# Kernel optimization log

Hardware: AMD Instinct MI355X
Metric: run time of the kernel (lower is better)

Reference implementation:

```python
import jax, jax.numpy as jnp
import numpy as np

N_NODES = 50000
N_EDGES = 1000000
D = 66
NEG_SLOPE = 0.2
EPS_BN = 1e-5


def _glorot(key, shape):
    fan = sum(shape)
    lim = jnp.sqrt(6.0 / fan)
    return jax.random.uniform(key, shape, jnp.float32, -lim, lim)


def setup_inputs() -> dict:
    key = jax.random.key(0)
    ks = jax.random.split(key, 40)
    inp = {
        'h': jax.random.normal(ks[0], (N_NODES, D), jnp.float32),
        'edge_index': jax.random.randint(ks[1], (2, N_EDGES), 0, N_NODES, jnp.int32),
        'edge_weight': jax.random.uniform(ks[2], (N_EDGES, 1), jnp.float32),
        'bn_gamma': jnp.ones((D,), jnp.float32),
        'bn_beta': jnp.zeros((D,), jnp.float32),
    }
    i = 3
    for l in (1, 2, 3):
        inp[f'W{l}'] = _glorot(ks[i], (D, D)); i += 1
        inp[f'b{l}'] = jnp.zeros((D,), jnp.float32)
        inp[f'att_src{l}'] = _glorot(ks[i], (D,)); i += 1
        inp[f'att_dst{l}'] = _glorot(ks[i], (D,)); i += 1
        inp[f'We{l}'] = _glorot(ks[i], (1, D)); i += 1
        inp[f'att_e{l}'] = _glorot(ks[i], (D,)); i += 1
    dims = [(D, D), (D, D), (D, D), (D, D), (D, 22)]
    for l, (din, dout) in enumerate(dims, start=1):
        inp[f'fc{l}_w'] = _glorot(ks[i], (din, dout)); i += 1
        inp[f'fc{l}_b'] = jnp.zeros((dout,), jnp.float32)
    return inp


def _gat_conv(h, src, dst, edge_weight, W, b, att_src, att_dst, We, att_e):
    x = h @ W                                     # [N, D]
    a_src = x @ att_src                           # [N]
    a_dst = x @ att_dst                           # [N]
    a_e = (edge_weight @ We) @ att_e              # [E]
    alpha = a_src[src] + a_dst[dst] + a_e         # [E]
    alpha = jnp.where(alpha > 0, alpha, NEG_SLOPE * alpha)
    # scatter-softmax over destination nodes
    m = jax.ops.segment_max(alpha, dst, num_segments=N_NODES)
    m = jnp.where(jnp.isfinite(m), m, 0.0)
    ex = jnp.exp(alpha - m[dst])
    denom = jax.ops.segment_sum(ex, dst, num_segments=N_NODES)
    coef = ex / (denom[dst] + 1e-16)              # [E]
    out = jax.ops.segment_sum(coef[:, None] * x[src], dst, num_segments=N_NODES)
    return out + b


def reference(h, edge_index, edge_weight, bn_gamma, bn_beta,
              W1, b1, att_src1, att_dst1, We1, att_e1,
              W2, b2, att_src2, att_dst2, We2, att_e2,
              W3, b3, att_src3, att_dst3, We3, att_e3,
              fc1_w, fc1_b, fc2_w, fc2_b, fc3_w, fc3_b,
              fc4_w, fc4_b, fc5_w, fc5_b):
    src, dst = edge_index[0], edge_index[1]
    # BatchNorm1d (training-mode batch statistics, biased variance)
    mean = h.mean(0)
    var = ((h - mean) ** 2).mean(0)
    x = (h - mean) * jax.lax.rsqrt(var + EPS_BN) * bn_gamma + bn_beta
    x = jax.nn.relu(_gat_conv(x, src, dst, edge_weight, W1, b1, att_src1, att_dst1, We1, att_e1))
    x = jax.nn.relu(_gat_conv(x, src, dst, edge_weight, W2, b2, att_src2, att_dst2, We2, att_e2))
    x = jax.nn.relu(_gat_conv(x, src, dst, edge_weight, W3, b3, att_src3, att_dst3, We3, att_e3))
    x = jax.nn.relu(x @ fc1_w + fc1_b)
    x = jax.nn.relu(x @ fc2_w + fc2_b)
    x = jax.nn.relu(x @ fc3_w + fc3_b)
    x = jax.nn.relu(x @ fc4_w + fc4_b)
    return x @ fc5_w + fc5_b
```

## Files before the change

### kernel.cpp

```cpp
#include <hip/hip_runtime.h>
#include <math.h>

#define D 66
#define SP 68
#define NEG_SLOPE 0.2f
#define CAP 6144

typedef short s8v __attribute__((ext_vector_type(8)));
typedef float f4v __attribute__((ext_vector_type(4)));

__device__ __forceinline__ float lrelu(float a){ return a > 0.f ? a : NEG_SLOPE * a; }
__device__ __forceinline__ void fma4(float4& a, float s, const float4& w){
  a.x = fmaf(s, w.x, a.x); a.y = fmaf(s, w.y, a.y);
  a.z = fmaf(s, w.z, a.z); a.w = fmaf(s, w.w, a.w);
}
__device__ __forceinline__ unsigned short bf16r(float f){
  unsigned u = __float_as_uint(f);
  u += 0x7FFFu + ((u >> 16) & 1u);
  return (unsigned short)(u >> 16);
}
__device__ __forceinline__ float bf16f(unsigned short b){
  return __uint_as_float(((unsigned)b) << 16);
}
__device__ __forceinline__ void split8(const float* p, s8v& a0, s8v& a1, s8v& a2){
  #pragma unroll
  for (int j = 0; j < 8; j++){
    float v = p[j];
    unsigned short b0 = bf16r(v);  float f0 = bf16f(b0);
    float r1 = v - f0;
    unsigned short b1 = bf16r(r1); float f1 = bf16f(b1);
    unsigned short b2 = bf16r(r1 - f1);
    a0[j] = (short)b0; a1[j] = (short)b1; a2[j] = (short)b2;
  }
}
#define MM6(acc, a0, a1, a2, b0v, b1v, b2v)                                \
  acc = __builtin_amdgcn_mfma_f32_16x16x32_bf16(a0, b0v, acc, 0, 0, 0);    \
  acc = __builtin_amdgcn_mfma_f32_16x16x32_bf16(a1, b0v, acc, 0, 0, 0);    \
  acc = __builtin_amdgcn_mfma_f32_16x16x32_bf16(a0, b1v, acc, 0, 0, 0);    \
  acc = __builtin_amdgcn_mfma_f32_16x16x32_bf16(a2, b0v, acc, 0, 0, 0);    \
  acc = __builtin_amdgcn_mfma_f32_16x16x32_bf16(a1, b1v, acc, 0, 0, 0);    \
  acc = __builtin_amdgcn_mfma_f32_16x16x32_bf16(a0, b2v, acc, 0, 0, 0);

__global__ __launch_bounds__(256) void k_bn_stats(const float* __restrict__ h,
                                                  float* __restrict__ sums, int n){
  __shared__ float ls[2 * D];
  int t = threadIdx.x;
  if (t < 2 * D) ls[t] = 0.f;
  __syncthreads();
  int rpb = (n + gridDim.x - 1) / gridDim.x;
  int r0 = blockIdx.x * rpb;
  int r1 = min(n, r0 + rpb);
  if (t < 3 * D){
    int c = t % D, seg = t / D;
    float s1 = 0.f, s2 = 0.f;
    for (int r = r0 + seg; r < r1; r += 3){
      float v = h[(size_t)r * D + c];
      s1 += v; s2 += v * v;
    }
    atomicAdd(&ls[c], s1);
    atomicAdd(&ls[D + c], s2);
  }
  __syncthreads();
  if (t < 2 * D) atomicAdd(&sums[t], ls[t]);
}

__global__ void k_bn_finalize(const float* __restrict__ sums,
                              const float* __restrict__ gamma, const float* __restrict__ beta,
                              const float* __restrict__ We1, const float* __restrict__ ae1,
                              const float* __restrict__ We2, const float* __restrict__ ae2,
                              const float* __restrict__ We3, const float* __restrict__ ae3,
                              float* __restrict__ misc, int n){
  int t = threadIdx.x;
  if (t < D){
    float mean = sums[t] / (float)n;
    float var  = sums[D + t] / (float)n - mean * mean;
    float inv  = rsqrtf(var + 1e-5f);
    float sc = gamma[t] * inv;
    misc[t] = sc;
    misc[D + t] = beta[t] - mean * sc;
  } else if (t == D){
    float c = 0.f; for (int d = 0; d < D; d++) c += We1[d] * ae1[d]; misc[2*D + 0] = c;
  } else if (t == D + 1){
    float c = 0.f; for (int d = 0; d < D; d++) c += We2[d] * ae2[d]; misc[2*D + 1] = c;
  } else if (t == D + 2){
    float c = 0.f; for (int d = 0; d < D; d++) c += We3[d] * ae3[d]; misc[2*D + 2] = c;
  }
}

__global__ __launch_bounds__(256) void k_bn_apply(const float* __restrict__ h, const float* __restrict__ misc,
                                                  float* __restrict__ x, int n){
  int i = blockIdx.x * 256 + threadIdx.x;
  int r = i / (SP/2), c2 = i - r * (SP/2);
  if (r >= n) return;
  int c = 2 * c2;
  float2 v = make_float2(0.f, 0.f);
  if (c < D){
    float2 hv = *(const float2*)&h[(size_t)r * D + c];
    v.x = hv.x * misc[c]     + misc[D + c];
    v.y = hv.y * misc[c + 1] + misc[D + c + 1];
  }
  *(float2*)&x[(size_t)r * SP + c] = v;
}

__global__ __launch_bounds__(256) void k_pack(const float* __restrict__ w0, const float* __restrict__ w1,
                                              const float* __restrict__ w2,
                                              short* __restrict__ W0, short* __restrict__ W1,
                                              short* __restrict__ W2){
  int tid = blockIdx.x * 256 + threadIdx.x;
  if (tid >= 3 * 15 * 64) return;
  int L = tid & 63;
  int ct = (tid >> 6) % 15;
  int lay = tid / 960;
  const float* w = (lay == 0) ? w0 : ((lay == 1) ? w1 : w2);
  int c = ct / 5, t = ct % 5;
  int nn = t * 16 + (L & 15);
  int kb = c * 32 + (L >> 4) * 8;
  #pragma unroll
  for (int j = 0; j < 8; j++){
    int k = kb + j;
    float v = (k < D && nn < D) ? w[k * D + nn] : 0.f;
    unsigned short b0 = bf16r(v);  float f0 = bf16f(b0);
    float r1 = v - f0;
    unsigned short b1 = bf16r(r1); float f1 = bf16f(b1);
    unsigned short b2 = bf16r(r1 - f1);
    W0[tid * 8 + j] = (short)b0;
    W1[tid * 8 + j] = (short)b1;
    W2[tid * 8 + j] = (short)b2;
  }
}

__global__ __launch_bounds__(256) void k_packfc(const float* __restrict__ w0, const float* __restrict__ w1,
                                                const float* __restrict__ w2, const float* __restrict__ w3,
                                                const float* __restrict__ w4,
                                                const float* __restrict__ b0, const float* __restrict__ b1,
                                                const float* __restrict__ b2, const float* __restrict__ b3,
                                                const float* __restrict__ b4,
                                                short* __restrict__ W0, short* __restrict__ W1,
                                                short* __restrict__ W2, float* __restrict__ bpack){
  int tid = blockIdx.x * 256 + threadIdx.x;
  if (tid < 5 * 15 * 64){
    int L = tid & 63;
    int ct = (tid >> 6) % 15;
    int lay = tid / 960;
    const float* w = (lay == 0) ? w0 : (lay == 1) ? w1 : (lay == 2) ? w2 : (lay == 3) ? w3 : w4;
    int ncol = (lay == 4) ? 22 : D;
    int c = ct / 5, t = ct % 5;
    int nn = t * 16 + (L & 15);
    int kb = c * 32 + (L >> 4) * 8;
    #pragma unroll
    for (int j = 0; j < 8; j++){
      int k = kb + j;
      float v = (k < D && nn < ncol) ? w[k * ncol + nn] : 0.f;
      unsigned short bb0 = bf16r(v);  float f0 = bf16f(bb0);
      float r1 = v - f0;
      unsigned short bb1 = bf16r(r1); float f1 = bf16f(bb1);
      unsigned short bb2 = bf16r(r1 - f1);
      W0[tid * 8 + j] = (short)bb0;
      W1[tid * 8 + j] = (short)bb1;
      W2[tid * 8 + j] = (short)bb2;
    }
  } else if (tid < 5 * 15 * 64 + 400){
    int i = tid - 5 * 15 * 64;
    int lay = i / 80, col = i % 80;
    const float* b = (lay == 0) ? b0 : (lay == 1) ? b1 : (lay == 2) ? b2 : (lay == 3) ? b3 : b4;
    int ncol = (lay == 4) ? 22 : D;
    bpack[i] = (col < ncol) ? b[col] : 0.f;
  }
}

__global__ __launch_bounds__(256) void k_hist(const int* __restrict__ dst,
                                              int* __restrict__ bhist, int E){
  __shared__ int h[256];
  int t = threadIdx.x;
  h[t] = 0;
  __syncthreads();
  int stride = gridDim.x * blockDim.x;
  for (int e = blockIdx.x * blockDim.x + t; e < E; e += stride)
    atomicAdd(&h[dst[e] >> 8], 1);
  __syncthreads();
  if (h[t]) atomicAdd(&bhist[t], h[t]);
}

__global__ void k_bscan(const int* __restrict__ bhist, int* __restrict__ bbase,
                        int* __restrict__ gcur, int* __restrict__ rowptr, int N, int E){
  __shared__ int sh[256];
  int t = threadIdx.x;
  int v = bhist[t];
  sh[t] = v; __syncthreads();
  for (int o = 1; o < 256; o <<= 1){
    int u = (t >= o) ? sh[t - o] : 0;
    __syncthreads();
    sh[t] += u;
    __syncthreads();
  }
  int ex = sh[t] - v;
  bbase[t] = ex;
  gcur[t] = ex;
  if (t == 255){ bbase[256] = sh[255]; rowptr[N] = E; }
}

#define PCHUNK 4096
__global__ __launch_bounds__(256) void k_part(const int* __restrict__ src, const int* __restrict__ dst,
                                              const float* __restrict__ ew,
                                              int* __restrict__ gcur, int2* __restrict__ tmp, int E){
  __shared__ int hist[256];
  __shared__ int base[256];
  int t = threadIdx.x;
  int e0 = blockIdx.x * PCHUNK;
  int eend = min(E, e0 + PCHUNK);
  hist[t] = 0;
  __syncthreads();
  for (int e = e0 + t; e < eend; e += 256)
    atomicAdd(&hist[dst[e] >> 8], 1);
  __syncthreads();
  if (hist[t] > 0) base[t] = atomicAdd(&gcur[t], hist[t]);
  hist[t] = 0;
  __syncthreads();
  for (int e = e0 + t; e < eend; e += 256){
    int d = dst[e];
    int b = d >> 8;
    int off = atomicAdd(&hist[b], 1);
    tmp[base[b] + off] = make_int2((src[e] & 0xffff) | ((d & 255) << 16), __float_as_int(ew[e]));
  }
}

__global__ __launch_bounds__(256) void k_bsort(const int2* __restrict__ tmp, const int* __restrict__ bbase,
                                               int2* __restrict__ epair, int* __restrict__ rowptr, int N){
  __shared__ int2 ebuf[CAP];
  __shared__ int lcnt[256];
  __shared__ int sc[256];
  __shared__ int lcur[256];
  int b = blockIdx.x, t = threadIdx.x;
  int s0 = bbase[b], s1 = bbase[b + 1];
  int cnt = s1 - s0;
  lcnt[t] = 0;
  __syncthreads();
  for (int j = t; j < cnt; j += 256){
    int2 e = tmp[s0 + j];
    if (j < CAP) ebuf[j] = e;
    atomicAdd(&lcnt[(e.x >> 16) & 255], 1);
  }
  __syncthreads();
  int v = lcnt[t];
  sc[t] = v; __syncthreads();
  for (int o = 1; o < 256; o <<= 1){
    int u = (t >= o) ? sc[t - o] : 0;
    __syncthreads();
    sc[t] += u;
    __syncthreads();
  }
  int ex = sc[t] - v;
  int node = (b << 8) + t;
  if (node < N) rowptr[node] = s0 + ex;
  lcur[t] = ex;
  __syncthreads();
  for (int j = t; j < cnt; j += 256){
    int2 e = (j < CAP) ? ebuf[j] : tmp[s0 + j];
    int i = (e.x >> 16) & 255;
    int p = atomicAdd(&lcur[i], 1);
    epair[s0 + p] = make_int2(e.x & 0xffff, e.y);
  }
}

__global__ __launch_bounds__(256) void k_mm(const float* __restrict__ X,
    const short* __restrict__ W0, const short* __restrict__ W1, const short* __restrict__ W2,
    const float* __restrict__ att_s, const float* __restrict__ att_d,
    float* __restrict__ Y, float* __restrict__ a_src, float* __restrict__ a_dst, int n){
  const int wv = threadIdx.x >> 6, L = threadIdx.x & 63;
  const int quad = L >> 4, m = L & 15;
  const int row0 = blockIdx.x * 64 + wv * 16;
  const int lrow = min(row0 + m, n - 1);
  const float* xr = X + (size_t)lrow * SP;
  f4v acc[5];
  #pragma unroll
  for (int t = 0; t < 5; t++) acc[t] = (f4v){0.f,0.f,0.f,0.f};

  #pragma unroll
  for (int c = 0; c < 3; c++){
    float xv[8];
    if (c < 2){
      float4 p0 = *(const float4*)&xr[c * 32 + quad * 8];
      float4 p1 = *(const float4*)&xr[c * 32 + quad * 8 + 4];
      xv[0] = p0.x; xv[1] = p0.y; xv[2] = p0.z; xv[3] = p0.w;
      xv[4] = p1.x; xv[5] = p1.y; xv[6] = p1.z; xv[7] = p1.w;
    } else {
      float4 p0 = make_float4(0.f, 0.f, 0.f, 0.f);
      if (quad == 0) p0 = *(const float4*)&xr[64];
      xv[0] = p0.x; xv[1] = p0.y; xv[2] = p0.z; xv[3] = p0.w;
      xv[4] = 0.f; xv[5] = 0.f; xv[6] = 0.f; xv[7] = 0.f;
    }
    s8v a0, a1, a2;
    split8(xv, a0, a1, a2);
    const short* b0p = W0 + (c * 5) * 512 + L * 8;
    const short* b1p = W1 + (c * 5) * 512 + L * 8;
    const short* b2p = W2 + (c * 5) * 512 + L * 8;
    #pragma unroll
    for (int t = 0; t < 5; t++){
      s8v b0v = *(const s8v*)(b0p + t * 512);
      s8v b1v = *(const s8v*)(b1p + t * 512);
      s8v b2v = *(const s8v*)(b2p + t * 512);
      MM6(acc[t], a0, a1, a2, b0v, b1v, b2v)
    }
  }

  float ps[4] = {0.f,0.f,0.f,0.f}, pd[4] = {0.f,0.f,0.f,0.f};
  #pragma unroll
  for (int t = 0; t < 5; t++){
    int col = t * 16 + m;
    float as_v = 0.f, ad_v = 0.f;
    if (col < D){ as_v = att_s[col]; ad_v = att_d[col]; }
    #pragma unroll
    for (int r = 0; r < 4; r++){
      ps[r] += acc[t][r] * as_v;
      pd[r] += acc[t][r] * ad_v;
    }
  }
  #pragma unroll
  for (int r = 0; r < 4; r++){
    int rw = row0 + quad * 4 + r;
    if (rw < n){
      float* yr = Y + (size_t)rw * SP;
      #pragma unroll
      for (int t = 0; t < 4; t++) yr[t * 16 + m] = acc[t][r];
      if (m < 4) yr[64 + m] = (m < 2) ? acc[4][r] : 0.f;
    }
  }
  #pragma unroll
  for (int o = 1; o <= 8; o <<= 1){
    #pragma unroll
    for (int r = 0; r < 4; r++){
      ps[r] += __shfl_xor(ps[r], o);
      pd[r] += __shfl_xor(pd[r], o);
    }
  }
  if (m == 0){
    #pragma unroll
    for (int r = 0; r < 4; r++){
      int rw = row0 + quad * 4 + r;
      if (rw < n){ a_src[rw] = ps[r]; a_dst[rw] = pd[r]; }
    }
  }
}

#define FST 84
__global__ __launch_bounds__(256) void k_fcmm(const float* __restrict__ X,
    const short* __restrict__ W0, const short* __restrict__ W1, const short* __restrict__ W2,
    const float* __restrict__ bpack, float* __restrict__ out, int n){
  __shared__ __align__(16) float xs[4][16][FST];
  const int wv = threadIdx.x >> 6, L = threadIdx.x & 63;
  const int quad = L >> 4, m = L & 15;
  const int row0 = blockIdx.x * 64 + wv * 16;
  const int lrow = min(row0 + m, n - 1);
  const float* xr = X + (size_t)lrow * SP;

  for (int l = 0; l < 5; l++){
    const int NTl = (l == 4) ? 2 : 5;
    f4v acc[5];
    #pragma unroll
    for (int t = 0; t < 5; t++) acc[t] = (f4v){0.f,0.f,0.f,0.f};
    #pragma unroll
    for (int c = 0; c < 3; c++){
      float xv[8];
      if (l == 0){
        if (c < 2){
          float4 p0 = *(const float4*)&xr[c * 32 + quad * 8];
          float4 p1 = *(const float4*)&xr[c * 32 + quad * 8 + 4];
          xv[0] = p0.x; xv[1] = p0.y; xv[2] = p0.z; xv[3] = p0.w;
          xv[4] = p1.x; xv[5] = p1.y; xv[6] = p1.z; xv[7] = p1.w;
        } else {
          float4 p0 = make_float4(0.f, 0.f, 0.f, 0.f);
          if (quad == 0) p0 = *(const float4*)&xr[64];
          xv[0] = p0.x; xv[1] = p0.y; xv[2] = p0.z; xv[3] = p0.w;
          xv[4] = 0.f; xv[5] = 0.f; xv[6] = 0.f; xv[7] = 0.f;
        }
      } else {
        if (c == 2 && quad >= 2){
          #pragma unroll
          for (int j = 0; j < 8; j++) xv[j] = 0.f;
        } else {
          float4 p0 = *(const float4*)&xs[wv][m][c * 32 + quad * 8];
          float4 p1 = *(const float4*)&xs[wv][m][c * 32 + quad * 8 + 4];
          xv[0] = p0.x; xv[1] = p0.y; xv[2] = p0.z; xv[3] = p0.w;
          xv[4] = p1.x; xv[5] = p1.y; xv[6] = p1.z; xv[7] = p1.w;
        }
      }
      s8v a0, a1, a2;
      split8(xv, a0, a1, a2);
      const short* b0p = W0 + ((l * 3 + c) * 5) * 512 + L * 8;
      const short* b1p = W1 + ((l * 3 + c) * 5) * 512 + L * 8;
      const short* b2p = W2 + ((l * 3 + c) * 5) * 512 + L * 8;
      for (int t = 0; t < NTl; t++){
        s8v b0v = *(const s8v*)(b0p + t * 512);
        s8v b1v = *(const s8v*)(b1p + t * 512);
        s8v b2v = *(const s8v*)(b2p + t * 512);
        MM6(acc[t], a0, a1, a2, b0v, b1v, b2v)
      }
    }
    if (l < 4){
      __syncthreads();
      #pragma unroll
      for (int t = 0; t < 5; t++){
        int col = t * 16 + m;
        float bv = bpack[l * 80 + col];
        #pragma unroll
        for (int r = 0; r < 4; r++){
          float v = acc[t][r] + bv;
          xs[wv][quad * 4 + r][col] = v > 0.f ? v : 0.f;
        }
      }
      __syncthreads();
    } else {
      #pragma unroll
      for (int t = 0; t < 2; t++){
        int col = t * 16 + m;
        #pragma unroll
        for (int r = 0; r < 4; r++){
          int rw = row0 + quad * 4 + r;
          if (col < 22 && rw < n) out[(size_t)rw * 22 + col] = acc[t][r] + bpack[4 * 80 + col];
        }
      }
    }
  }
}

__global__ __launch_bounds__(256) void k_agg(const float* __restrict__ y,
                                             const float* __restrict__ a_src, const float* __restrict__ a_dst,
                                             const int* __restrict__ rowptr, const int2* __restrict__ epair,
                                             const float* __restrict__ misc, int cidx,
                                             const float* __restrict__ bias,
                                             float* __restrict__ xout, int n){
  const int wid  = (int)((blockIdx.x * (size_t)blockDim.x + threadIdx.x) >> 6);
  const int lane = threadIdx.x & 63;
  if (wid >= n) return;
  const int beg = rowptr[wid];
  const int deg = rowptr[wid + 1] - beg;
  const float ce  = misc[2 * D + cidx];
  const float adn = a_dst[wid];
  const int g = lane >> 3, q = lane & 7;

  float4 accA = make_float4(0.f,0.f,0.f,0.f);
  float4 accB = make_float4(0.f,0.f,0.f,0.f);
  float2 tacc = make_float2(0.f,0.f);

  if (deg <= 64){
    int s = 0; float al = -INFINITY;
    bool act = lane < deg;
    if (act){
      int2 ep = epair[beg + lane];
      s = ep.x;
      al = lrelu(a_src[s] + adn + ce * __int_as_float(ep.y));
    }
    float mx = al;
    #pragma unroll
    for (int o = 32; o; o >>= 1) mx = fmaxf(mx, __shfl_xor(mx, o));
    float ex = act ? __expf(al - mx) : 0.f;
    float sum = ex;
    #pragma unroll
    for (int o = 32; o; o >>= 1) sum += __shfl_xor(sum, o);
    float coef = ex * (1.f / (sum + 1e-16f));
    for (int e0 = 0; e0 < deg; e0 += 8){
      int e = e0 + g;
      int   st = __shfl(s, e);
      float ct = __shfl(coef, e);
      if (e < deg){
        const float* row = y + (size_t)st * SP;
        float4 y0 = *(const float4*)&row[4 * q];
        float4 y1 = *(const float4*)&row[32 + 4 * q];
        fma4(accA, ct, y0);
        fma4(accB, ct, y1);
        if (q == 0){
          float2 tv = *(const float2*)&row[64];
          tacc.x += ct * tv.x; tacc.y += ct * tv.y;
        }
      }
    }
  } else {
    float mx = -INFINITY;
    for (int j0 = 0; j0 < deg; j0 += 64){
      int j = j0 + lane;
      if (j < deg){
        int2 ep = epair[beg + j];
        mx = fmaxf(mx, lrelu(a_src[ep.x] + adn + ce * __int_as_float(ep.y)));
      }
    }
    #pragma unroll
    for (int o = 32; o; o >>= 1) mx = fmaxf(mx, __shfl_xor(mx, o));
    float sum = 0.f;
    for (int j0 = 0; j0 < deg; j0 += 64){
      int j = j0 + lane;
      if (j < deg){
        int2 ep = epair[beg + j];
        sum += __expf(lrelu(a_src[ep.x] + adn + ce * __int_as_float(ep.y)) - mx);
      }
    }
    #pragma unroll
    for (int o = 32; o; o >>= 1) sum += __shfl_xor(sum, o);
    float inv = 1.f / (sum + 1e-16f);
    for (int j0 = 0; j0 < deg; j0 += 64){
      int cnt = min(64, deg - j0);
      int s = 0; float ex = 0.f;
      if (lane < cnt){
        int2 ep = epair[beg + j0 + lane];
        s = ep.x;
        ex = __expf(lrelu(a_src[s] + adn + ce * __int_as_float(ep.y)) - mx);
      }
      float coef = ex * inv;
      for (int e0 = 0; e0 < cnt; e0 += 8){
        int e = e0 + g;
        int   st = __shfl(s, e);
        float ct = __shfl(coef, e);
        if (e < cnt){
          const float* row = y + (size_t)st * SP;
          float4 y0 = *(const float4*)&row[4 * q];
          float4 y1 = *(const float4*)&row[32 + 4 * q];
          fma4(accA, ct, y0);
          fma4(accB, ct, y1);
          if (q == 0){
            float2 tv = *(const float2*)&row[64];
            tacc.x += ct * tv.x; tacc.y += ct * tv.y;
          }
        }
      }
    }
  }

  #pragma unroll
  for (int o = 8; o <= 32; o <<= 1){
    accA.x += __shfl_xor(accA.x, o); accA.y += __shfl_xor(accA.y, o);
    accA.z += __shfl_xor(accA.z, o); accA.w += __shfl_xor(accA.w, o);
    accB.x += __shfl_xor(accB.x, o); accB.y += __shfl_xor(accB.y, o);
    accB.z += __shfl_xor(accB.z, o); accB.w += __shfl_xor(accB.w, o);
    tacc.x += __shfl_xor(tacc.x, o); tacc.y += __shfl_xor(tacc.y, o);
  }
  float* orow = xout + (size_t)wid * SP;
  if (lane < 8){
    float4 v;
    v.x = accA.x + bias[4*lane+0]; v.x = v.x > 0.f ? v.x : 0.f;
    v.y = accA.y + bias[4*lane+1]; v.y = v.y > 0.f ? v.y : 0.f;
    v.z = accA.z + bias[4*lane+2]; v.z = v.z > 0.f ? v.z : 0.f;
    v.w = accA.w + bias[4*lane+3]; v.w = v.w > 0.f ? v.w : 0.f;
    *(float4*)&orow[4 * lane] = v;
  } else if (lane < 16){
    int qq = lane - 8;
    float4 v;
    v.x = accB.x + bias[32+4*qq+0]; v.x = v.x > 0.f ? v.x : 0.f;
    v.y = accB.y + bias[32+4*qq+1]; v.y = v.y > 0.f ? v.y : 0.f;
    v.z = accB.z + bias[32+4*qq+2]; v.z = v.z > 0.f ? v.z : 0.f;
    v.w = accB.w + bias[32+4*qq+3]; v.w = v.w > 0.f ? v.w : 0.f;
    *(float4*)&orow[32 + 4 * qq] = v;
  }
  if (lane == 0){
    float4 tv;
    tv.x = tacc.x + bias[64]; tv.x = tv.x > 0.f ? tv.x : 0.f;
    tv.y = tacc.y + bias[65]; tv.y = tv.y > 0.f ? tv.y : 0.f;
    tv.z = 0.f; tv.w = 0.f;
    *(float4*)&orow[64] = tv;
  }
}

extern "C" void kernel_launch(void* const* d_in, const int* in_sizes, int n_in,
                              void* d_out, int out_size, void* d_ws, size_t ws_size,
                              hipStream_t stream){
  const float* h     = (const float*)d_in[0];
  const int*   ei    = (const int*)  d_in[1];
  const float* ew    = (const float*)d_in[2];
  const float* gamma = (const float*)d_in[3];
  const float* beta  = (const float*)d_in[4];
  const float *Wl[3], *bl[3], *asl[3], *adl[3], *Wel[3], *ael[3];
  int idx = 5;
  for (int l = 0; l < 3; l++){
    Wl[l]  = (const float*)d_in[idx++];
    bl[l]  = (const float*)d_in[idx++];
    asl[l] = (const float*)d_in[idx++];
    adl[l] = (const float*)d_in[idx++];
    Wel[l] = (const float*)d_in[idx++];
    ael[l] = (const float*)d_in[idx++];
  }
  const float *fw[5], *fb[5];
  for (int l = 0; l < 5; l++){ fw[l] = (const float*)d_in[idx++]; fb[l] = (const float*)d_in[idx++]; }

  int N = in_sizes[0] / D;
  int E = in_sizes[1] / 2;
  const int* src  = ei;
  const int* dstp = ei + E;

  char* base = (char*)d_ws;
  size_t o = 0;
  auto alloc = [&](size_t b){ size_t r = o; o += (b + 255) & ~(size_t)255; return r; };
  float*  bufA   = (float*)(base + alloc((size_t)N * SP * 4));
  float*  bufB   = (float*)(base + alloc((size_t)N * SP * 4));
  float*  a_src  = (float*)(base + alloc((size_t)N * 4));
  float*  a_dst  = (float*)(base + alloc((size_t)N * 4));
  float*  misc   = (float*)(base + alloc(512 * 4));
  float*  sums   = (float*)(base + alloc(2 * D * 4));
  int*    rowptr = (int*)  (base + alloc((size_t)(N + 1) * 4));
  int*    bhist  = (int*)  (base + alloc(256 * 4));
  int*    bbase  = (int*)  (base + alloc(257 * 4));
  int*    gcur   = (int*)  (base + alloc(256 * 4));
  int2*   epair  = (int2*) (base + alloc((size_t)E * 8));
  short*  W0p    = (short*)(base + alloc(3 * 7680 * 2));
  short*  W1p    = (short*)(base + alloc(3 * 7680 * 2));
  short*  W2p    = (short*)(base + alloc(3 * 7680 * 2));
  short*  FW0p   = (short*)(base + alloc(5 * 7680 * 2));
  short*  FW1p   = (short*)(base + alloc(5 * 7680 * 2));
  short*  FW2p   = (short*)(base + alloc(5 * 7680 * 2));
  float*  bpack  = (float*)(base + alloc(400 * 4));
  int2*   tmp    = (int2*)bufB;

  hipMemsetAsync(sums, 0, 2 * D * 4, stream);
  hipMemsetAsync(bhist, 0, 256 * 4, stream);

  k_bn_stats<<<256, 256, 0, stream>>>(h, sums, N);
  k_bn_finalize<<<1, 128, 0, stream>>>(sums, gamma, beta, Wel[0], ael[0], Wel[1], ael[1], Wel[2], ael[2], misc, N);
  k_pack<<<12, 256, 0, stream>>>(Wl[0], Wl[1], Wl[2], W0p, W1p, W2p);
  k_packfc<<<21, 256, 0, stream>>>(fw[0], fw[1], fw[2], fw[3], fw[4],
                                   fb[0], fb[1], fb[2], fb[3], fb[4],
                                   FW0p, FW1p, FW2p, bpack);

  int NB = (N + 255) >> 8;
  k_hist<<<256, 256, 0, stream>>>(dstp, bhist, E);
  k_bscan<<<1, 256, 0, stream>>>(bhist, bbase, gcur, rowptr, N, E);
  k_part<<<(E + PCHUNK - 1) / PCHUNK, 256, 0, stream>>>(src, dstp, ew, gcur, tmp, E);
  k_bsort<<<NB, 256, 0, stream>>>(tmp, bbase, epair, rowptr, N);

  int bnb = ((size_t)N * (SP/2) + 255) / 256;
  k_bn_apply<<<bnb, 256, 0, stream>>>(h, misc, bufA, N);

  int gb = (N + 63) / 64;
  int ab = (N + 3) / 4;

  for (int l = 0; l < 3; l++){
    k_mm<<<gb, 256, 0, stream>>>(bufA, W0p + l * 7680, W1p + l * 7680, W2p + l * 7680,
                                 asl[l], adl[l], bufB, a_src, a_dst, N);
    k_agg<<<ab, 256, 0, stream>>>(bufB, a_src, a_dst, rowptr, epair, misc, l, bl[l], bufA, N);
  }

  k_fcmm<<<gb, 256, 0, stream>>>(bufA, FW0p, FW1p, FW2p, bpack, (float*)d_out, N);
}
```

Baseline: 475.4 us.

## Fuse prep kernels, fold BatchNorm into first matmul, truncate-split activations

BN stats and the dst histogram now run as one launch, and BN finalize plus both weight-packing steps share a single prep kernel, which removes several small launches. The BN apply kernel is gone; the first GAT matmul reads raw h and applies the scale and shift inline, so one full pass over the node features is no longer written and re-read. Activations are split into three bf16 parts by truncation instead of round-to-nearest, which needs fewer ALU ops but leaves larger residuals for the lower parts. In the FC kernel the block barriers around the per-wave shared-memory exchange become a compiler memory fence, which relies on each wave touching only its own slice.

```diff
diff --git a/kernel.cpp b/kernel.cpp
--- a/kernel.cpp
+++ b/kernel.cpp
@@ -22,15 +22,18 @@
 __device__ __forceinline__ float bf16f(unsigned short b){
   return __uint_as_float(((unsigned)b) << 16);
 }
-__device__ __forceinline__ void split8(const float* p, s8v& a0, s8v& a1, s8v& a2){
+__device__ __forceinline__ void split8t(const float* p, s8v& a0, s8v& a1, s8v& a2){
   #pragma unroll
   for (int j = 0; j < 8; j++){
     float v = p[j];
-    unsigned short b0 = bf16r(v);  float f0 = bf16f(b0);
-    float r1 = v - f0;
-    unsigned short b1 = bf16r(r1); float f1 = bf16f(b1);
-    unsigned short b2 = bf16r(r1 - f1);
-    a0[j] = (short)b0; a1[j] = (short)b1; a2[j] = (short)b2;
+    unsigned u0 = __float_as_uint(v) & 0xFFFF0000u;
+    float r1 = v - __uint_as_float(u0);
+    unsigned u1 = __float_as_uint(r1) & 0xFFFF0000u;
+    float r2 = r1 - __uint_as_float(u1);
+    unsigned u2 = __float_as_uint(r2);
+    a0[j] = (short)(u0 >> 16);
+    a1[j] = (short)(u1 >> 16);
+    a2[j] = (short)(u2 >> 16);
   }
 }
 #define MM6(acc, a0, a1, a2, b0v, b1v, b2v)                                \
@@ -41,144 +44,118 @@
   acc = __builtin_amdgcn_mfma_f32_16x16x32_bf16(a1, b1v, acc, 0, 0, 0);    \
   acc = __builtin_amdgcn_mfma_f32_16x16x32_bf16(a0, b2v, acc, 0, 0, 0);
 
-__global__ __launch_bounds__(256) void k_bn_stats(const float* __restrict__ h,
-                                                  float* __restrict__ sums, int n){
-  __shared__ float ls[2 * D];
+__global__ __launch_bounds__(256) void k_stats_hist(const float* __restrict__ h, const int* __restrict__ dst,
+                                                    float* __restrict__ sums, int* __restrict__ bhist,
+                                                    int n, int E){
   int t = threadIdx.x;
-  if (t < 2 * D) ls[t] = 0.f;
-  __syncthreads();
-  int rpb = (n + gridDim.x - 1) / gridDim.x;
-  int r0 = blockIdx.x * rpb;
-  int r1 = min(n, r0 + rpb);
-  if (t < 3 * D){
-    int c = t % D, seg = t / D;
-    float s1 = 0.f, s2 = 0.f;
-    for (int r = r0 + seg; r < r1; r += 3){
-      float v = h[(size_t)r * D + c];
-      s1 += v; s2 += v * v;
-    }
-    atomicAdd(&ls[c], s1);
-    atomicAdd(&ls[D + c], s2);
-  }
-  __syncthreads();
-  if (t < 2 * D) atomicAdd(&sums[t], ls[t]);
-}
-
-__global__ void k_bn_finalize(const float* __restrict__ sums,
-                              const float* __restrict__ gamma, const float* __restrict__ beta,
-                              const float* __restrict__ We1, const float* __restrict__ ae1,
-                              const float* __restrict__ We2, const float* __restrict__ ae2,
-                              const float* __restrict__ We3, const float* __restrict__ ae3,
-                              float* __restrict__ misc, int n){
+  if (blockIdx.x < 256){
+    __shared__ float ls[2 * D];
+    if (t < 2 * D) ls[t] = 0.f;
+    __syncthreads();
+    int rpb = (n + 255) / 256;
+    int r0 = blockIdx.x * rpb;
+    int r1 = min(n, r0 + rpb);
+    if (t < 3 * D){
+      int c = t % D, seg = t / D;
+      float s1 = 0.f, s2 = 0.f;
+      for (int r = r0 + seg; r < r1; r += 3){
+        float v = h[(size_t)r * D + c];
+        s1 += v; s2 += v * v;
+      }
+      atomicAdd(&ls[c], s1);
+      atomicAdd(&ls[D + c], s2);
+    }
+    __syncthreads();
+    if (t < 2 * D) atomicAdd(&sums[t], ls[t]);
+  } else {
+    __shared__ int hh[256];
+    hh[t] = 0;
+    __syncthreads();
+    int stride = 256 * 256;
+    for (int e = (blockIdx.x - 256) * 256 + t; e < E; e += stride)
+      atomicAdd(&hh[dst[e] >> 8], 1);
+    __syncthreads();
+    if (hh[t]) atomicAdd(&bhist[t], hh[t]);
+  }
+}
+
+struct PrepArgs {
+  const float *sums, *gamma, *beta;
+  const float *We[3], *ae[3];
+  const float *gw[3];
+  const float *fw[5], *fb[5];
+  float *misc; short *W0, *W1, *W2; short *F0, *F1, *F2; float *bpack;
+  int n;
+};
+
+__global__ __launch_bounds__(256) void k_prep(PrepArgs pa){
   int t = threadIdx.x;
-  if (t < D){
-    float mean = sums[t] / (float)n;
-    float var  = sums[D + t] / (float)n - mean * mean;
-    float inv  = rsqrtf(var + 1e-5f);
-    float sc = gamma[t] * inv;
-    misc[t] = sc;
-    misc[D + t] = beta[t] - mean * sc;
-  } else if (t == D){
-    float c = 0.f; for (int d = 0; d < D; d++) c += We1[d] * ae1[d]; misc[2*D + 0] = c;
-  } else if (t == D + 1){
-    float c = 0.f; for (int d = 0; d < D; d++) c += We2[d] * ae2[d]; misc[2*D + 1] = c;
-  } else if (t == D + 2){
-    float c = 0.f; for (int d = 0; d < D; d++) c += We3[d] * ae3[d]; misc[2*D + 2] = c;
-  }
-}
-
-__global__ __launch_bounds__(256) void k_bn_apply(const float* __restrict__ h, const float* __restrict__ misc,
-                                                  float* __restrict__ x, int n){
-  int i = blockIdx.x * 256 + threadIdx.x;
-  int r = i / (SP/2), c2 = i - r * (SP/2);
-  if (r >= n) return;
-  int c = 2 * c2;
-  float2 v = make_float2(0.f, 0.f);
-  if (c < D){
-    float2 hv = *(const float2*)&h[(size_t)r * D + c];
-    v.x = hv.x * misc[c]     + misc[D + c];
-    v.y = hv.y * misc[c + 1] + misc[D + c + 1];
-  }
-  *(float2*)&x[(size_t)r * SP + c] = v;
-}
-
-__global__ __launch_bounds__(256) void k_pack(const float* __restrict__ w0, const float* __restrict__ w1,
-                                              const float* __restrict__ w2,
-                                              short* __restrict__ W0, short* __restrict__ W1,
-                                              short* __restrict__ W2){
-  int tid = blockIdx.x * 256 + threadIdx.x;
-  if (tid >= 3 * 15 * 64) return;
-  int L = tid & 63;
-  int ct = (tid >> 6) % 15;
-  int lay = tid / 960;
-  const float* w = (lay == 0) ? w0 : ((lay == 1) ? w1 : w2);
-  int c = ct / 5, t = ct % 5;
-  int nn = t * 16 + (L & 15);
-  int kb = c * 32 + (L >> 4) * 8;
-  #pragma unroll
-  for (int j = 0; j < 8; j++){
-    int k = kb + j;
-    float v = (k < D && nn < D) ? w[k * D + nn] : 0.f;
-    unsigned short b0 = bf16r(v);  float f0 = bf16f(b0);
-    float r1 = v - f0;
-    unsigned short b1 = bf16r(r1); float f1 = bf16f(b1);
-    unsigned short b2 = bf16r(r1 - f1);
-    W0[tid * 8 + j] = (short)b0;
-    W1[tid * 8 + j] = (short)b1;
-    W2[tid * 8 + j] = (short)b2;
-  }
-}
-
-__global__ __launch_bounds__(256) void k_packfc(const float* __restrict__ w0, const float* __restrict__ w1,
-                                                const float* __restrict__ w2, const float* __restrict__ w3,
-                                                const float* __restrict__ w4,
-                                                const float* __restrict__ b0, const float* __restrict__ b1,
-                                                const float* __restrict__ b2, const float* __restrict__ b3,
-                                                const float* __restrict__ b4,
-                                                short* __restrict__ W0, short* __restrict__ W1,
-                                                short* __restrict__ W2, float* __restrict__ bpack){
-  int tid = blockIdx.x * 256 + threadIdx.x;
-  if (tid < 5 * 15 * 64){
+  if (blockIdx.x == 0){
+    if (t < D){
+      float mean = pa.sums[t] / (float)pa.n;
+      float var  = pa.sums[D + t] / (float)pa.n - mean * mean;
+      float inv  = rsqrtf(var + 1e-5f);
+      float sc = pa.gamma[t] * inv;
+      pa.misc[t] = sc;
+      pa.misc[D + t] = pa.beta[t] - mean * sc;
+    } else if (t >= D && t < D + 3){
+      int l = t - D;
+      float c = 0.f;
+      for (int d = 0; d < D; d++) c += pa.We[l][d] * pa.ae[l][d];
+      pa.misc[2 * D + l] = c;
+    }
+  } else if (blockIdx.x <= 12){
+    int tid = (blockIdx.x - 1) * 256 + t;
+    if (tid >= 3 * 960) return;
     int L = tid & 63;
     int ct = (tid >> 6) % 15;
     int lay = tid / 960;
-    const float* w = (lay == 0) ? w0 : (lay == 1) ? w1 : (lay == 2) ? w2 : (lay == 3) ? w3 : w4;
-    int ncol = (lay == 4) ? 22 : D;
-    int c = ct / 5, t = ct % 5;
-    int nn = t * 16 + (L & 15);
+    const float* w = pa.gw[lay];
+    int c = ct / 5, tt = ct % 5;
+    int nn = tt * 16 + (L & 15);
     int kb = c * 32 + (L >> 4) * 8;
     #pragma unroll
     for (int j = 0; j < 8; j++){
       int k = kb + j;
-      float v = (k < D && nn < ncol) ? w[k * ncol + nn] : 0.f;
-      unsigned short bb0 = bf16r(v);  float f0 = bf16f(bb0);
+      float v = (k < D && nn < D) ? w[k * D + nn] : 0.f;
+      unsigned short b0 = bf16r(v);  float f0 = bf16f(b0);
       float r1 = v - f0;
-      unsigned short bb1 = bf16r(r1); float f1 = bf16f(bb1);
-      unsigned short bb2 = bf16r(r1 - f1);
-      W0[tid * 8 + j] = (short)bb0;
-      W1[tid * 8 + j] = (short)bb1;
-      W2[tid * 8 + j] = (short)bb2;
-    }
-  } else if (tid < 5 * 15 * 64 + 400){
-    int i = tid - 5 * 15 * 64;
-    int lay = i / 80, col = i % 80;
-    const float* b = (lay == 0) ? b0 : (lay == 1) ? b1 : (lay == 2) ? b2 : (lay == 3) ? b3 : b4;
-    int ncol = (lay == 4) ? 22 : D;
-    bpack[i] = (col < ncol) ? b[col] : 0.f;
-  }
-}
-
-__global__ __launch_bounds__(256) void k_hist(const int* __restrict__ dst,
-                                              int* __restrict__ bhist, int E){
-  __shared__ int h[256];
-  int t = threadIdx.x;
-  h[t] = 0;
-  __syncthreads();
-  int stride = gridDim.x * blockDim.x;
-  for (int e = blockIdx.x * blockDim.x + t; e < E; e += stride)
-    atomicAdd(&h[dst[e] >> 8], 1);
-  __syncthreads();
-  if (h[t]) atomicAdd(&bhist[t], h[t]);
+      unsigned short b1 = bf16r(r1); float f1 = bf16f(b1);
+      unsigned short b2 = bf16r(r1 - f1);
+      pa.W0[tid * 8 + j] = (short)b0;
+      pa.W1[tid * 8 + j] = (short)b1;
+      pa.W2[tid * 8 + j] = (short)b2;
+    }
+  } else {
+    int tid = (blockIdx.x - 13) * 256 + t;
+    if (tid < 5 * 960){
+      int L = tid & 63;
+      int ct = (tid >> 6) % 15;
+      int lay = tid / 960;
+      const float* w = pa.fw[lay];
+      int ncol = (lay == 4) ? 22 : D;
+      int c = ct / 5, tt = ct % 5;
+      int nn = tt * 16 + (L & 15);
+      int kb = c * 32 + (L >> 4) * 8;
+      #pragma unroll
+      for (int j = 0; j < 8; j++){
+        int k = kb + j;
+        float v = (k < D && nn < ncol) ? w[k * ncol + nn] : 0.f;
+        unsigned short b0 = bf16r(v);  float f0 = bf16f(b0);
+        float r1 = v - f0;
+        unsigned short b1 = bf16r(r1); float f1 = bf16f(b1);
+        unsigned short b2 = bf16r(r1 - f1);
+        pa.F0[tid * 8 + j] = (short)b0;
+        pa.F1[tid * 8 + j] = (short)b1;
+        pa.F2[tid * 8 + j] = (short)b2;
+      }
+    } else if (tid < 5 * 960 + 400){
+      int i = tid - 5 * 960;
+      int lay = i / 80, col = i % 80;
+      int ncol = (lay == 4) ? 22 : D;
+      pa.bpack[i] = (col < ncol) ? pa.fb[lay][col] : 0.f;
+    }
+  }
 }
 
 __global__ void k_bscan(const int* __restrict__ bhist, int* __restrict__ bbase,
@@ -262,15 +239,16 @@
   }
 }
 
+template<bool BN_IN>
 __global__ __launch_bounds__(256) void k_mm(const float* __restrict__ X,
     const short* __restrict__ W0, const short* __restrict__ W1, const short* __restrict__ W2,
     const float* __restrict__ att_s, const float* __restrict__ att_d,
+    const float* __restrict__ bn,
     float* __restrict__ Y, float* __restrict__ a_src, float* __restrict__ a_dst, int n){
   const int wv = threadIdx.x >> 6, L = threadIdx.x & 63;
   const int quad = L >> 4, m = L & 15;
   const int row0 = blockIdx.x * 64 + wv * 16;
   const int lrow = min(row0 + m, n - 1);
-  const float* xr = X + (size_t)lrow * SP;
   f4v acc[5];
   #pragma unroll
   for (int t = 0; t < 5; t++) acc[t] = (f4v){0.f,0.f,0.f,0.f};
@@ -279,18 +257,38 @@
   for (int c = 0; c < 3; c++){
     float xv[8];
     if (c < 2){
-      float4 p0 = *(const float4*)&xr[c * 32 + quad * 8];
-      float4 p1 = *(const float4*)&xr[c * 32 + quad * 8 + 4];
-      xv[0] = p0.x; xv[1] = p0.y; xv[2] = p0.z; xv[3] = p0.w;
-      xv[4] = p1.x; xv[5] = p1.y; xv[6] = p1.z; xv[7] = p1.w;
+      if (BN_IN){
+        const float* hr = X + (size_t)lrow * D + c * 32 + quad * 8;
+        #pragma unroll
+        for (int j = 0; j < 8; j += 2){
+          float2 hv = *(const float2*)(hr + j);
+          int col = c * 32 + quad * 8 + j;
+          xv[j]     = hv.x * bn[col]     + bn[D + col];
+          xv[j + 1] = hv.y * bn[col + 1] + bn[D + col + 1];
+        }
+      } else {
+        const float* xr = X + (size_t)lrow * SP;
+        float4 p0 = *(const float4*)&xr[c * 32 + quad * 8];
+        float4 p1 = *(const float4*)&xr[c * 32 + quad * 8 + 4];
+        xv[0] = p0.x; xv[1] = p0.y; xv[2] = p0.z; xv[3] = p0.w;
+        xv[4] = p1.x; xv[5] = p1.y; xv[6] = p1.z; xv[7] = p1.w;
+      }
     } else {
-      float4 p0 = make_float4(0.f, 0.f, 0.f, 0.f);
-      if (quad == 0) p0 = *(const float4*)&xr[64];
-      xv[0] = p0.x; xv[1] = p0.y; xv[2] = p0.z; xv[3] = p0.w;
-      xv[4] = 0.f; xv[5] = 0.f; xv[6] = 0.f; xv[7] = 0.f;
+      #pragma unroll
+      for (int j = 0; j < 8; j++) xv[j] = 0.f;
+      if (quad == 0){
+        if (BN_IN){
+          float2 hv = *(const float2*)(X + (size_t)lrow * D + 64);
+          xv[0] = hv.x * bn[64] + bn[D + 64];
+          xv[1] = hv.y * bn[65] + bn[D + 65];
+        } else {
+          float4 p0 = *(const float4*)&X[(size_t)lrow * SP + 64];
+          xv[0] = p0.x; xv[1] = p0.y; xv[2] = p0.z; xv[3] = p0.w;
+        }
+      }
     }
     s8v a0, a1, a2;
-    split8(xv, a0, a1, a2);
+    split8t(xv, a0, a1, a2);
     const short* b0p = W0 + (c * 5) * 512 + L * 8;
     const short* b1p = W1 + (c * 5) * 512 + L * 8;
     const short* b2p = W2 + (c * 5) * 512 + L * 8;
@@ -385,7 +383,7 @@
         }
       }
       s8v a0, a1, a2;
-      split8(xv, a0, a1, a2);
+      split8t(xv, a0, a1, a2);
       const short* b0p = W0 + ((l * 3 + c) * 5) * 512 + L * 8;
       const short* b1p = W1 + ((l * 3 + c) * 5) * 512 + L * 8;
       const short* b2p = W2 + ((l * 3 + c) * 5) * 512 + L * 8;
@@ -397,7 +395,6 @@
       }
     }
     if (l < 4){
-      __syncthreads();
       #pragma unroll
       for (int t = 0; t < 5; t++){
         int col = t * 16 + m;
@@ -408,7 +405,7 @@
           xs[wv][quad * 4 + r][col] = v > 0.f ? v : 0.f;
         }
       }
-      __syncthreads();
+      __asm__ volatile("" ::: "memory");
     } else {
       #pragma unroll
       for (int t = 0; t < 2; t++){
@@ -610,30 +607,33 @@
   hipMemsetAsync(sums, 0, 2 * D * 4, stream);
   hipMemsetAsync(bhist, 0, 256 * 4, stream);
 
-  k_bn_stats<<<256, 256, 0, stream>>>(h, sums, N);
-  k_bn_finalize<<<1, 128, 0, stream>>>(sums, gamma, beta, Wel[0], ael[0], Wel[1], ael[1], Wel[2], ael[2], misc, N);
-  k_pack<<<12, 256, 0, stream>>>(Wl[0], Wl[1], Wl[2], W0p, W1p, W2p);
-  k_packfc<<<21, 256, 0, stream>>>(fw[0], fw[1], fw[2], fw[3], fw[4],
-                                   fb[0], fb[1], fb[2], fb[3], fb[4],
-                                   FW0p, FW1p, FW2p, bpack);
+  k_stats_hist<<<512, 256, 0, stream>>>(h, dstp, sums, bhist, N, E);
+
+  PrepArgs pa;
+  pa.sums = sums; pa.gamma = gamma; pa.beta = beta;
+  for (int l = 0; l < 3; l++){ pa.We[l] = Wel[l]; pa.ae[l] = ael[l]; pa.gw[l] = Wl[l]; }
+  for (int l = 0; l < 5; l++){ pa.fw[l] = fw[l]; pa.fb[l] = fb[l]; }
+  pa.misc = misc; pa.W0 = W0p; pa.W1 = W1p; pa.W2 = W2p;
+  pa.F0 = FW0p; pa.F1 = FW1p; pa.F2 = FW2p; pa.bpack = bpack; pa.n = N;
+  k_prep<<<34, 256, 0, stream>>>(pa);
 
   int NB = (N + 255) >> 8;
-  k_hist<<<256, 256, 0, stream>>>(dstp, bhist, E);
   k_bscan<<<1, 256, 0, stream>>>(bhist, bbase, gcur, rowptr, N, E);
   k_part<<<(E + PCHUNK - 1) / PCHUNK, 256, 0, stream>>>(src, dstp, ew, gcur, tmp, E);
   k_bsort<<<NB, 256, 0, stream>>>(tmp, bbase, epair, rowptr, N);
 
-  int bnb = ((size_t)N * (SP/2) + 255) / 256;
-  k_bn_apply<<<bnb, 256, 0, stream>>>(h, misc, bufA, N);
-
   int gb = (N + 63) / 64;
   int ab = (N + 3) / 4;
 
-  for (int l = 0; l < 3; l++){
-    k_mm<<<gb, 256, 0, stream>>>(bufA, W0p + l * 7680, W1p + l * 7680, W2p + l * 7680,
-                                 asl[l], adl[l], bufB, a_src, a_dst, N);
-    k_agg<<<ab, 256, 0, stream>>>(bufB, a_src, a_dst, rowptr, epair, misc, l, bl[l], bufA, N);
-  }
+  k_mm<true ><<<gb, 256, 0, stream>>>(h,    W0p + 0 * 7680, W1p + 0 * 7680, W2p + 0 * 7680,
+                                      asl[0], adl[0], misc, bufB, a_src, a_dst, N);
+  k_agg<<<ab, 256, 0, stream>>>(bufB, a_src, a_dst, rowptr, epair, misc, 0, bl[0], bufA, N);
+  k_mm<false><<<gb, 256, 0, stream>>>(bufA, W0p + 1 * 7680, W1p + 1 * 7680, W2p + 1 * 7680,
+                                      asl[1], adl[1], misc, bufB, a_src, a_dst, N);
+  k_agg<<<ab, 256, 0, stream>>>(bufB, a_src, a_dst, rowptr, epair, misc, 1, bl[1], bufA, N);
+  k_mm<false><<<gb, 256, 0, stream>>>(bufA, W0p + 2 * 7680, W1p + 2 * 7680, W2p + 2 * 7680,
+                                      asl[2], adl[2], misc, bufB, a_src, a_dst, N);
+  k_agg<<<ab, 256, 0, stream>>>(bufB, a_src, a_dst, rowptr, epair, misc, 2, bl[2], bufA, N);
 
   k_fcmm<<<gb, 256, 0, stream>>>(bufA, FW0p, FW1p, FW2p, bpack, (float*)d_out, N);
 }
```

After: 445.5 us. 1.07x faster.
